# Performance work log

Hardware: AMD Instinct MI355X
Metric: run time of the kernel (lower is better)

The kernel has to match this reference:

```python
import jax, jax.numpy as jnp
import numpy as np

B, IN_CHS, P = 512, 200, 19
CF, TF, K, D, NC = 64, 32, 48, 32, 16
BN_EPS = 1e-5


def _conv(x, w, b=None, dil=1):
    y = jax.lax.conv_general_dilated(x, w, (1, 1), 'VALID',
                                     rhs_dilation=(dil, dil),
                                     dimension_numbers=('NCHW', 'OIHW', 'NCHW'))
    if b is not None:
        y = y + b[None, :, None, None]
    return y


def _upsample_bilinear_ac(x, oh, ow):
    # bilinear with align_corners=True (torch UpsamplingBilinear2d)
    N, C, H, W = x.shape
    ys = jnp.linspace(0.0, H - 1.0, oh)
    xs = jnp.linspace(0.0, W - 1.0, ow)
    y0 = jnp.floor(ys).astype(jnp.int32)
    y1 = jnp.minimum(y0 + 1, H - 1)
    x0 = jnp.floor(xs).astype(jnp.int32)
    x1 = jnp.minimum(x0 + 1, W - 1)
    wy = (ys - y0.astype(ys.dtype))[None, None, :, None]
    wx = (xs - x0.astype(xs.dtype))[None, None, None, :]
    rows = x[:, :, y0, :] * (1.0 - wy) + x[:, :, y1, :] * wy
    return rows[:, :, :, x0] * (1.0 - wx) + rows[:, :, :, x1] * wx


def setup_inputs() -> dict:
    key = jax.random.key(0)
    ks = jax.random.split(key, 24)
    std1 = 1.0 / np.sqrt(K * D)
    inp = {
        'x': jax.random.normal(ks[0], (B, IN_CHS, P, P), jnp.float32),
        'w0': jax.random.normal(ks[1], (CF, IN_CHS, 3, 3), jnp.float32) * 0.02,
        'b0': jnp.zeros((CF,), jnp.float32),
        'w1': jax.random.normal(ks[2], (CF, CF, 3, 3), jnp.float32) * 0.05,
        'b1': jnp.zeros((CF,), jnp.float32),
        'w2': jax.random.normal(ks[3], (CF, CF, 3, 3), jnp.float32) * 0.05,
        'b2': jnp.zeros((CF,), jnp.float32),
        'wa': jax.random.normal(ks[4], (TF, CF, 1, 1), jnp.float32) * 0.08,
        'wb': jax.random.normal(ks[5], (TF, CF, 1, 1), jnp.float32) * 0.08,
        'wg': jax.random.normal(ks[6], (TF, CF, 1, 1), jnp.float32) * 0.08,
        'wd': jax.random.normal(ks[7], (CF, TF, 1, 1), jnp.float32) * 0.08,
        'wenc': jax.random.normal(ks[8], (D, CF, 1, 1), jnp.float32) * 0.08,
        'codewords': jax.random.uniform(ks[9], (K, D), jnp.float32, -std1, std1),
        'scale': jax.random.uniform(ks[10], (K,), jnp.float32, -1.0, 0.0),
        'w_att': jax.random.normal(ks[11], (CF, D), jnp.float32) * 0.1,
        'b_att': jnp.zeros((CF,), jnp.float32),
        'bn_g': jnp.ones((K,), jnp.float32),
        'bn_b': jnp.zeros((K,), jnp.float32),
        'w_d1': jax.random.normal(ks[12], (256, 3 * CF * P * P), jnp.float32) * 0.004,
        'b_d1': jnp.zeros((256,), jnp.float32),
        'w_d2': jax.random.normal(ks[13], (128, 256), jnp.float32) * 0.06,
        'b_d2': jnp.zeros((128,), jnp.float32),
        'w_d3': jax.random.normal(ks[14], (NC, 128), jnp.float32) * 0.09,
        'b_d3': jnp.zeros((NC,), jnp.float32),
    }
    return inp


def reference(x, w0, b0, w1, b1, w2, b2, wa, wb, wg, wd, wenc,
              codewords, scale, w_att, b_att, bn_g, bn_b,
              w_d1, b_d1, w_d2, b_d2, w_d3, b_d3):
    relu = jax.nn.relu
    Hin, Win = x.shape[2], x.shape[3]
    c1 = relu(_conv(x, w0, b0, 1))        # (b, CF, 17, 17)
    c2 = relu(_conv(c1, w1, b1, 2))       # (b, CF, 13, 13)
    xx = relu(_conv(c2, w2, b2, 3))       # (b, CF, 7, 7)
    n, c, h, w = xx.shape
    hw = h * w
    # non-local block; alpha view(n,-1,TF) is a RAW reshape in torch (not a transpose)
    alpha = _conv(xx, wa).reshape(n, hw, TF)
    beta = _conv(xx, wb).reshape(n, TF, hw)
    gam = relu(_conv(xx, wg)).reshape(n, TF, hw)
    ctx = jnp.matmul(alpha, beta)                 # (n, hw, hw)
    ctx = jax.nn.softmax(ctx, axis=0)             # torch F.softmax default dim for 3D tensor is 0
    ctx = jnp.matmul(gam, ctx).reshape(n, TF, h, w)
    ctx = _upsample_bilinear_ac(ctx, h, w)        # same-size -> identity, kept for fidelity
    xx = relu(_conv(ctx, wd)) + xx
    # soft VQ encoding
    Z = relu(_conv(xx, wenc)).reshape(n, D, hw).transpose(0, 2, 1)   # (b, hw, D)
    dist = scale * (jnp.sum(Z * Z, -1, keepdims=True)
                    + jnp.sum(codewords * codewords, -1)[None, None, :]
                    - 2.0 * jnp.einsum('bnd,kd->bnk', Z, codewords))  # (b, hw, K)
    A = jax.nn.softmax(dist, axis=2)
    # E[b,k,d] = sum_n A[b,n,k] * (Z[b,n,d] - C[k,d])
    E = jnp.einsum('bnk,bnd->bkd', A, Z) - A.sum(1)[:, :, None] * codewords[None]
    # BatchNorm1d(K) in training mode: stats over (batch, D) per code k
    mu = E.mean(axis=(0, 2), keepdims=True)
    var = E.var(axis=(0, 2), keepdims=True)
    En = relu((E - mu) / jnp.sqrt(var + BN_EPS) * bn_g[None, :, None] + bn_b[None, :, None])
    E_sum = En.sum(1)                              # (b, D)
    gate = jax.nn.sigmoid(E_sum @ w_att.T + b_att)  # (b, CF)
    xx = xx + xx * gate[:, :, None, None]
    ctx3 = _upsample_bilinear_ac(xx, Hin, Win)
    c2u = _upsample_bilinear_ac(c2, Hin, Win)
    c1u = _upsample_bilinear_ac(c1, Hin, Win)
    feat = jnp.concatenate((c1u, c2u, ctx3), axis=1).reshape(n, -1)  # (b, 69312)
    h1 = relu(feat @ w_d1.T + b_d1)
    h2 = relu(h1 @ w_d2.T + b_d2)
    return h2 @ w_d3.T + b_d3
```

## Files before the change

### kernel.cpp

```cpp
#include <hip/hip_runtime.h>
#include <math.h>


typedef __attribute__((ext_vector_type(8))) short short8v;
typedef __attribute__((ext_vector_type(4))) float f32x4;

#define OFF_WE1H  188928u
#define OFF_WE1L  2556416u
#define OFF_WE2H  4923904u
#define OFF_WE2L  6308352u
#define OFF_WE3H  7692800u
#define OFF_WE3L  8094208u
#define OFF_C1    8495616u
#define OFF_C2    17965568u
#define OFF_XX1   23503360u
#define OFF_ALPHA 25108992u
#define OFF_BETA  25911808u
#define OFF_GAM   26714624u
#define OFF_CTX   27517440u
#define OFF_CTX2  28746752u
#define OFF_XX2   29549568u
#define OFF_Z     31155200u
#define OFF_A     31958016u
#define OFF_E     33162240u
#define OFF_BNS   33948672u
#define OFF_XX3   33948768u
#define OFF_H1    35554400u
#define OFF_H2    35685472u

#define OFF_H1P   OFF_ALPHA
#define OFF_MS    OFF_BETA

#define OFF_WH    OFF_ALPHA
#define OFF_WL    (OFF_ALPHA + 64512u)
#define OFF_W1H   (OFF_ALPHA + 129024u)
#define OFF_W1L   (OFF_W1H + 18432u)
#define OFF_W2H   (OFF_W1L + 18432u)
#define OFF_W2L   (OFF_W2H + 18432u)

__device__ __forceinline__ unsigned bf16_rne_bits(float v) {
    unsigned u = __float_as_uint(v);
    return (u + 0x7FFFu + ((u >> 16) & 1u)) >> 16;
}

__global__ __launch_bounds__(256) void sac_wsplit(const float* __restrict__ w0,
                                                  unsigned short* __restrict__ WH,
                                                  unsigned short* __restrict__ WL) {
    int idx = blockIdx.x * 256 + threadIdx.x;
    if (idx >= 129024) return;
    int ic = idx % 224;
    int c  = (idx / 224) % 64;
    int s  = idx / (224 * 64);
    int ky = s / 3, kx = s % 3;
    float v = 0.f;
    if (ic < 200) v = w0[((c * 200 + ic) * 3 + ky) * 3 + kx];
    unsigned hb = bf16_rne_bits(v);
    float hf = __uint_as_float(hb << 16);
    unsigned lb = bf16_rne_bits(v - hf);
    WH[idx] = (unsigned short)hb;
    WL[idx] = (unsigned short)lb;
}

__global__ __launch_bounds__(256) void sac_wsplit64(const float* __restrict__ wsrc,
                                                    unsigned short* __restrict__ WHo,
                                                    unsigned short* __restrict__ WLo) {
    int idx = blockIdx.x * 256 + threadIdx.x;
    if (idx >= 36864) return;
    int ic = idx & 63;
    int c  = (idx >> 6) & 63;
    int s  = idx >> 12;
    int ky = s / 3, kx = s - ky * 3;
    float v = wsrc[((c * 64 + ic) * 3 + ky) * 3 + kx];
    unsigned hb = bf16_rne_bits(v);
    float hf = __uint_as_float(hb << 16);
    unsigned lb = bf16_rne_bits(v - hf);
    WHo[idx] = (unsigned short)hb;
    WLo[idx] = (unsigned short)lb;
}

__global__ __launch_bounds__(256) void sac_upA(const float* __restrict__ w_d1,
                                               float* __restrict__ tmp, int S, int co) {
    int idx = blockIdx.x * 256 + threadIdx.x;
    int total = 256 * 64 * 19 * S;
    if (idx >= total) return;
    int xp = idx % S;
    int j  = (idx / S) % 19;
    int c  = (idx / (S * 19)) % 64;
    int o  = idx / (S * 19 * 64);
    const float* wrow = w_d1 + (size_t)o * 69312 + (size_t)(co + c) * 361 + j * 19;
    float ratio = (float)(S - 1) / 18.0f;
    float s = 0.f;
    for (int i = 0; i < 19; ++i) {
        float xs = i * ratio;
        int x0 = (int)floorf(xs);
        float wx = xs - (float)x0;
        int x1 = x0 + 1; if (x1 > S - 1) x1 = S - 1;
        float cf = (xp == x0 ? 1.f - wx : 0.f) + (xp == x1 ? wx : 0.f);
        s += cf * wrow[i];
    }
    tmp[idx] = s;
}
__global__ __launch_bounds__(256) void sac_upB_bf16(const float* __restrict__ tmp,
                                                    unsigned short* __restrict__ WEH,
                                                    unsigned short* __restrict__ WEL, int S) {
    int idx = blockIdx.x * 256 + threadIdx.x;
    int total = 256 * 64 * S * S;
    if (idx >= total) return;
    int xp = idx % S;
    int yp = (idx / S) % S;
    int c  = (idx / (S * S)) % 64;
    int o  = idx / (S * S * 64);
    const float* tp = tmp + (((size_t)o * 64 + c) * 19) * S + xp;
    float ratio = (float)(S - 1) / 18.0f;
    float s = 0.f;
    for (int j = 0; j < 19; ++j) {
        float ys = j * ratio;
        int y0 = (int)floorf(ys);
        float wy = ys - (float)y0;
        int y1 = y0 + 1; if (y1 > S - 1) y1 = S - 1;
        float cf = (yp == y0 ? 1.f - wy : 0.f) + (yp == y1 ? wy : 0.f);
        s += cf * tp[j * S];
    }
    unsigned hb = bf16_rne_bits(s);
    float hf = __uint_as_float(hb << 16);
    unsigned lb = bf16_rne_bits(s - hf);
    WEH[idx] = (unsigned short)hb;
    WEL[idx] = (unsigned short)lb;
}

template<int IW, int OW, int DIL, int TOTCH, int WSTR, int NMT, int NIRMAX>
__global__ __launch_bounds__(256, 4) void sac_convmfma(const float* __restrict__ x,
                                                       const unsigned short* __restrict__ WHp,
                                                       const unsigned short* __restrict__ WLp,
                                                       const float* __restrict__ bias,
                                                       float* __restrict__ out) {
    constexpr int OP = OW * OW;
    constexpr int ISZ = IW * IW;
    constexpr int NCHUNK = WSTR / 32;
    constexpr int NRC = NIRMAX * IW;
    constexpr int RB = (NRC + 31) / 32;
    __shared__ __align__(16) unsigned short XH[NRC * 32 + 64];
    __shared__ __align__(16) unsigned short XL[NRC * 32 + 64];
    int blk = blockIdx.x;
    int b = blk / NMT, mt = blk - b * NMT;
    int tid = threadIdx.x;
    int wv = tid >> 6, l = tid & 63;
    int lh = l >> 5, li = l & 31;
    int wm = wv >> 1, wn = wv & 1;
    int q = l >> 4, r = l & 15;
    int p_base = mt * 64 + wm * 32;
    int n_base = wn * 32;
    int pixA = p_base + r;      if (pixA > OP - 1) pixA = OP - 1;
    int pixB = p_base + 16 + r; if (pixB > OP - 1) pixB = OP - 1;
    int pyA = pixA / OW, pxa = pixA - pyA * OW;
    int pyB = pixB / OW, pxb = pixB - pyB * OW;
    int ir0 = (mt * 64) / OW;
    int rcA0 = (pyA - ir0) * IW + pxa;
    int rcB0 = (pyB - ir0) * IW + pxb;

    f32x4 acc[2][2];
    #pragma unroll
    for (int i = 0; i < 2; ++i)
        #pragma unroll
        for (int j = 0; j < 2; ++j) { acc[i][j].x = 0.f; acc[i][j].y = 0.f; acc[i][j].z = 0.f; acc[i][j].w = 0.f; }

    for (int cc = 0; cc < NCHUNK; ++cc) {
        int ch0 = cc * 32;
        __syncthreads();
        for (int it = wv; it < 4 * RB; it += 4) {
            int cg = it / RB, rb = it - cg * RB;
            int rc = rb * 32 + li;
            if (rc < NRC) {
                int chl4 = cg * 2 + lh;
                int ch = ch0 + chl4 * 4;
                int idx = ir0 * IW + rc; if (idx > ISZ - 1) idx = ISZ - 1;
                const float* gp = x + (size_t)b * (TOTCH * ISZ) + (size_t)ch * ISZ + idx;
                float v0 = (ch + 0 < TOTCH) ? gp[0] : 0.f;
                float v1 = (ch + 1 < TOTCH) ? gp[ISZ] : 0.f;
                float v2 = (ch + 2 < TOTCH) ? gp[2 * ISZ] : 0.f;
                float v3 = (ch + 3 < TOTCH) ? gp[3 * ISZ] : 0.f;
                unsigned h0 = bf16_rne_bits(v0); unsigned l0 = bf16_rne_bits(v0 - __uint_as_float(h0 << 16));
                unsigned h1 = bf16_rne_bits(v1); unsigned l1 = bf16_rne_bits(v1 - __uint_as_float(h1 << 16));
                unsigned h2 = bf16_rne_bits(v2); unsigned l2 = bf16_rne_bits(v2 - __uint_as_float(h2 << 16));
                unsigned h3 = bf16_rne_bits(v3); unsigned l3 = bf16_rne_bits(v3 - __uint_as_float(h3 << 16));
                unsigned bo = ((unsigned)(rc * 64 + chl4 * 8)) ^ (unsigned)((rc & 7) << 4);
                uint2 hv; hv.x = h0 | (h1 << 16); hv.y = h2 | (h3 << 16);
                uint2 lv; lv.x = l0 | (l1 << 16); lv.y = l2 | (l3 << 16);
                *(uint2*)((char*)XH + bo) = hv;
                *(uint2*)((char*)XL + bo) = lv;
            }
        }
        __syncthreads();
        #pragma unroll 3
        for (int s9 = 0; s9 < 9; ++s9) {
            int ky = s9 / 3, kx = s9 - ky * 3;
            int rcA = rcA0 + DIL * (ky * IW + kx);
            int rcB = rcB0 + DIL * (ky * IW + kx);
            unsigned byA = ((unsigned)(rcA * 64 + q * 16)) ^ (unsigned)((rcA & 7) << 4);
            unsigned byB = ((unsigned)(rcB * 64 + q * 16)) ^ (unsigned)((rcB & 7) << 4);
            short8v ah0 = *(const short8v*)((const char*)XH + byA);
            short8v al0 = *(const short8v*)((const char*)XL + byA);
            short8v ah1 = *(const short8v*)((const char*)XH + byB);
            short8v al1 = *(const short8v*)((const char*)XL + byB);
            const unsigned short* pWH = WHp + (size_t)(s9 * 64 + n_base + r) * WSTR + ch0 + q * 8;
            const unsigned short* pWL = WLp + (size_t)(s9 * 64 + n_base + r) * WSTR + ch0 + q * 8;
            short8v bh0 = *(const short8v*)(pWH);
            short8v bh1 = *(const short8v*)(pWH + 16 * WSTR);
            short8v bl0 = *(const short8v*)(pWL);
            short8v bl1 = *(const short8v*)(pWL + 16 * WSTR);
            acc[0][0] = __builtin_amdgcn_mfma_f32_16x16x32_bf16(ah0, bh0, acc[0][0], 0, 0, 0);
            acc[0][1] = __builtin_amdgcn_mfma_f32_16x16x32_bf16(ah0, bh1, acc[0][1], 0, 0, 0);
            acc[1][0] = __builtin_amdgcn_mfma_f32_16x16x32_bf16(ah1, bh0, acc[1][0], 0, 0, 0);
            acc[1][1] = __builtin_amdgcn_mfma_f32_16x16x32_bf16(ah1, bh1, acc[1][1], 0, 0, 0);
            acc[0][0] = __builtin_amdgcn_mfma_f32_16x16x32_bf16(ah0, bl0, acc[0][0], 0, 0, 0);
            acc[0][1] = __builtin_amdgcn_mfma_f32_16x16x32_bf16(ah0, bl1, acc[0][1], 0, 0, 0);
            acc[1][0] = __builtin_amdgcn_mfma_f32_16x16x32_bf16(ah1, bl0, acc[1][0], 0, 0, 0);
            acc[1][1] = __builtin_amdgcn_mfma_f32_16x16x32_bf16(ah1, bl1, acc[1][1], 0, 0, 0);
            acc[0][0] = __builtin_amdgcn_mfma_f32_16x16x32_bf16(al0, bh0, acc[0][0], 0, 0, 0);
            acc[0][1] = __builtin_amdgcn_mfma_f32_16x16x32_bf16(al0, bh1, acc[0][1], 0, 0, 0);
            acc[1][0] = __builtin_amdgcn_mfma_f32_16x16x32_bf16(al1, bh0, acc[1][0], 0, 0, 0);
            acc[1][1] = __builtin_amdgcn_mfma_f32_16x16x32_bf16(al1, bh1, acc[1][1], 0, 0, 0);
        }
    }
    float bias0 = bias[n_base + r];
    float bias1 = bias[n_base + 16 + r];
    #pragma unroll
    for (int mf = 0; mf < 2; ++mf) {
        #pragma unroll
        for (int nf = 0; nf < 2; ++nf) {
            int ch = n_base + nf * 16 + r;
            float bs = nf ? bias1 : bias0;
            float* op = out + ((size_t)b * 64 + ch) * OP;
            #pragma unroll
            for (int j = 0; j < 4; ++j) {
                int pix = p_base + mf * 16 + q * 4 + j;
                if (pix < OP) {
                    float v = acc[mf][nf][j] + bs;
                    op[pix] = v > 0.f ? v : 0.f;
                }
            }
        }
    }
}

__global__ __launch_bounds__(256) void sac_abgctx(const float* __restrict__ xx1,
                                                  const float* __restrict__ wa,
                                                  const float* __restrict__ wb,
                                                  const float* __restrict__ wg,
                                                  float* __restrict__ gam,
                                                  float* __restrict__ ctx) {
    int b = blockIdx.x, tid = threadIdx.x;
    __shared__ float xsm[3136];
    __shared__ float ws3[3 * 2048];
    __shared__ float ab[3136];
    for (int f = tid; f < 3136; f += 256) xsm[f] = xx1[(size_t)b * 3136 + f];
    for (int f = tid; f < 2048; f += 256) {
        ws3[f] = wa[f]; ws3[2048 + f] = wb[f]; ws3[4096 + f] = wg[f];
    }
    __syncthreads();
    for (int f = tid; f < 4704; f += 256) {
        int which = f / 1568, r = f - which * 1568;
        int t = r / 49, p = r - t * 49;
        const float* w = &ws3[which * 2048 + t * 64];
        float s = 0.f;
        #pragma unroll 8
        for (int c = 0; c < 64; ++c) s += w[c] * xsm[c * 49 + p];
        if (which == 2) {
            s = s > 0.f ? s : 0.f;
            gam[(size_t)b * 1568 + r] = s;
        } else {
            ab[which * 1568 + r] = s;
        }
    }
    __syncthreads();
    for (int f = tid; f < 2401; f += 256) {
        int i = f / 49, lcol = f - i * 49;
        float s = 0.f;
        #pragma unroll 8
        for (int j = 0; j < 32; ++j) s += ab[i * 32 + j] * ab[1568 + j * 49 + lcol];
        ctx[(size_t)b * 2401 + f] = s;
    }
}

__global__ __launch_bounds__(256) void sac_smstat(const float* __restrict__ ctx,
                                                  float* __restrict__ ms) {
    __shared__ float red[8][32];
    int tid = threadIdx.x;
    int pl = tid & 31, g = tid >> 5;
    int pos = blockIdx.x * 32 + pl;
    bool ok = pos < 2401;
    float m = -1e30f;
    if (ok) for (int b = g; b < 512; b += 8) m = fmaxf(m, ctx[(size_t)b * 2401 + pos]);
    red[g][pl] = m;
    __syncthreads();
    if (g == 0) {
        #pragma unroll
        for (int t = 1; t < 8; ++t) m = fmaxf(m, red[t][pl]);
        red[0][pl] = m;
    }
    __syncthreads();
    m = red[0][pl];
    float s = 0.f;
    if (ok) for (int b = g; b < 512; b += 8) s += expf(ctx[(size_t)b * 2401 + pos] - m);
    __syncthreads();
    red[g][pl] = s;
    __syncthreads();
    if (g == 0 && ok) {
        #pragma unroll
        for (int t = 1; t < 8; ++t) s += red[t][pl];
        ms[pos] = m;
        ms[2401 + pos] = 1.f / s;
    }
}

__global__ __launch_bounds__(256) void sac_ctx2(const float* __restrict__ gam,
                                                const float* __restrict__ ctx,
                                                const float* __restrict__ ms,
                                                float* __restrict__ ctx2) {
    int b = blockIdx.x, tid = threadIdx.x;
    __shared__ float gs[1568];
    __shared__ float cs[2401];
    for (int f = tid; f < 1568; f += 256) gs[f] = gam[(size_t)b * 1568 + f];
    for (int f = tid; f < 2401; f += 256)
        cs[f] = expf(ctx[(size_t)b * 2401 + f] - ms[f]) * ms[2401 + f];
    __syncthreads();
    for (int f = tid; f < 1568; f += 256) {
        int t = f / 49, lcol = f - t * 49;
        float s = 0.f;
        #pragma unroll 7
        for (int i = 0; i < 49; ++i) s += gs[t * 49 + i] * cs[i * 49 + lcol];
        ctx2[(size_t)b * 1568 + f] = s;
    }
}

__global__ __launch_bounds__(256) void sac_xx2z(const float* __restrict__ ctx2,
                                                const float* __restrict__ wd,
                                                const float* __restrict__ xx1,
                                                const float* __restrict__ wenc,
                                                float* __restrict__ xx2,
                                                float* __restrict__ Z) {
    int b = blockIdx.x, tid = threadIdx.x;
    __shared__ float cs[1568];
    __shared__ float wds[2048];
    __shared__ float xs2[3136];
    __shared__ float wt[2048];
    for (int f = tid; f < 1568; f += 256) cs[f] = ctx2[(size_t)b * 1568 + f];
    for (int f = tid; f < 2048; f += 256) {
        wds[f] = wd[f];
        int d = f >> 6, c = f & 63; wt[c * 32 + d] = wenc[f];
    }
    __syncthreads();
    for (int f = tid; f < 3136; f += 256) {
        int c = f / 49, p = f - c * 49;
        float s = 0.f;
        #pragma unroll 8
        for (int t = 0; t < 32; ++t) s += wds[c * 32 + t] * cs[t * 49 + p];
        s = s > 0.f ? s : 0.f;
        s += xx1[(size_t)b * 3136 + f];
        xs2[f] = s;
        xx2[(size_t)b * 3136 + f] = s;
    }
    __syncthreads();
    for (int f = tid; f < 1568; f += 256) {
        int p = f >> 5, d = f & 31;
        float s = 0.f;
        #pragma unroll 8
        for (int c = 0; c < 64; ++c) s += wt[c * 32 + d] * xs2[c * 49 + p];
        Z[(size_t)b * 1568 + f] = s > 0.f ? s : 0.f;
    }
}

__global__ __launch_bounds__(256) void sac_dista(const float* __restrict__ Z,
                                                 const float* __restrict__ cw,
                                                 const float* __restrict__ scale,
                                                 float* __restrict__ A) {
    __shared__ float cws[1536];
    __shared__ float c2s[48];
    __shared__ float scs[48];
    int tid = threadIdx.x;
    for (int f = tid; f < 1536; f += 256) cws[f] = cw[f];
    if (tid < 48) scs[tid] = scale[tid];
    __syncthreads();
    if (tid < 48) {
        float s = 0.f;
        for (int d = 0; d < 32; ++d) { float v = cws[tid * 32 + d]; s += v * v; }
        c2s[tid] = s;
    }
    __syncthreads();
    int idx = blockIdx.x * 256 + tid;
    if (idx >= 25088) return;
    const float4* zp = (const float4*)(Z + (size_t)idx * 32);
    float zr[32];
    #pragma unroll
    for (int q = 0; q < 8; ++q) {
        float4 v = zp[q];
        zr[q * 4] = v.x; zr[q * 4 + 1] = v.y; zr[q * 4 + 2] = v.z; zr[q * 4 + 3] = v.w;
    }
    float z2 = 0.f;
    #pragma unroll
    for (int d = 0; d < 32; ++d) z2 += zr[d] * zr[d];
    float v48[48];
    float m = -1e30f;
    for (int k = 0; k < 48; ++k) {
        float dot = 0.f;
        #pragma unroll
        for (int d = 0; d < 32; ++d) dot += zr[d] * cws[k * 32 + d];
        float dv = scs[k] * (z2 + c2s[k] - 2.f * dot);
        v48[k] = dv;
        m = fmaxf(m, dv);
    }
    float s = 0.f;
    #pragma unroll
    for (int k = 0; k < 48; ++k) { v48[k] = expf(v48[k] - m); s += v48[k]; }
    float inv = 1.f / s;
    float* ap = A + (size_t)idx * 48;
    #pragma unroll
    for (int k = 0; k < 48; ++k) ap[k] = v48[k] * inv;
}

__global__ __launch_bounds__(256) void sac_e(const float* __restrict__ A,
                                             const float* __restrict__ Z,
                                             const float* __restrict__ cw,
                                             float* __restrict__ E) {
    int b = blockIdx.x, tid = threadIdx.x;
    __shared__ float As[2352];
    __shared__ float Zs[1568];
    __shared__ float asum[48];
    for (int f = tid; f < 2352; f += 256) As[f] = A[(size_t)b * 2352 + f];
    for (int f = tid; f < 1568; f += 256) Zs[f] = Z[(size_t)b * 1568 + f];
    __syncthreads();
    if (tid < 48) {
        float s = 0.f;
        for (int p = 0; p < 49; ++p) s += As[p * 48 + tid];
        asum[tid] = s;
    }
    __syncthreads();
    for (int f = tid; f < 1536; f += 256) {
        int k = f >> 5, d = f & 31;
        float s = 0.f;
        #pragma unroll 7
        for (int p = 0; p < 49; ++p) s += As[p * 48 + k] * Zs[p * 32 + d];
        E[(size_t)b * 1536 + f] = s - asum[k] * cw[f];
    }
}

__global__ __launch_bounds__(256) void sac_bnstat(const float* __restrict__ E,
                                                  float* __restrict__ bns) {
    int k = blockIdx.x, tid = threadIdx.x;
    __shared__ float sr[4];
    float s = 0.f;
    for (int i = tid; i < 16384; i += 256) {
        int b = i >> 5, d = i & 31;
        s += E[((size_t)b * 48 + k) * 32 + d];
    }
    #pragma unroll
    for (int off = 32; off > 0; off >>= 1) s += __shfl_xor(s, off, 64);
    int lane = tid & 63, wid = tid >> 6;
    if (lane == 0) sr[wid] = s;
    __syncthreads();
    float mu = (sr[0] + sr[1] + sr[2] + sr[3]) / 16384.f;
    float q = 0.f;
    for (int i = tid; i < 16384; i += 256) {
        int b = i >> 5, d = i & 31;
        float v = E[((size_t)b * 48 + k) * 32 + d] - mu;
        q += v * v;
    }
    #pragma unroll
    for (int off = 32; off > 0; off >>= 1) q += __shfl_xor(q, off, 64);
    __syncthreads();
    if (lane == 0) sr[wid] = q;
    __syncthreads();
    if (tid == 0) {
        float var = (sr[0] + sr[1] + sr[2] + sr[3]) / 16384.f;
        bns[k] = mu;
        bns[48 + k] = rsqrtf(var + 1e-5f);
    }
}

__global__ __launch_bounds__(256) void sac_gate(const float* __restrict__ E,
                                                const float* __restrict__ bns,
                                                const float* __restrict__ bn_g,
                                                const float* __restrict__ bn_b,
                                                const float* __restrict__ w_att,
                                                const float* __restrict__ b_att,
                                                const float* __restrict__ xx2,
                                                float* __restrict__ xx3) {
    int b = blockIdx.x, tid = threadIdx.x;
    __shared__ float esd[32];
    __shared__ float gs[64];
    if (tid < 32) {
        int d = tid;
        float s = 0.f;
        for (int k = 0; k < 48; ++k) {
            float v = (E[((size_t)b * 48 + k) * 32 + d] - bns[k]) * bns[48 + k] * bn_g[k] + bn_b[k];
            s += v > 0.f ? v : 0.f;
        }
        esd[d] = s;
    }
    __syncthreads();
    if (tid < 64) {
        int c = tid;
        float a = b_att[c];
        #pragma unroll 8
        for (int d = 0; d < 32; ++d) a += esd[d] * w_att[c * 32 + d];
        gs[c] = 1.f / (1.f + expf(-a)) + 1.f;
    }
    __syncthreads();
    for (int f = tid; f < 3136; f += 256) {
        int c = f / 49;
        xx3[(size_t)b * 3136 + f] = xx2[(size_t)b * 3136 + f] * gs[c];
    }
}

__global__ __launch_bounds__(256, 4) void sac_d1gemm_mfma(const float* __restrict__ c1,
                                                          const float* __restrict__ c2,
                                                          const float* __restrict__ xx3,
                                                          const unsigned short* __restrict__ we1h,
                                                          const unsigned short* __restrict__ we1l,
                                                          const unsigned short* __restrict__ we2h,
                                                          const unsigned short* __restrict__ we2l,
                                                          const unsigned short* __restrict__ we3h,
                                                          const unsigned short* __restrict__ we3l,
                                                          float* __restrict__ h1p) {
    constexpr int KCH = 128;
    __shared__ unsigned short AH[64 * KCH + 64];
    int blk = blockIdx.x;
    int g = blk >> 5, r5 = blk & 31;
    int b0 = (r5 >> 2) * 64, o0 = (r5 & 3) * 64;
    const float* Ab; const unsigned short *WHb, *WLb; int astr, klen, kbase;
    if (g < 16)      { int slab = g >> 2, kq4 = g & 3;
                       Ab = c1;  WHb = we1h; WLb = we1l; astr = 18496; klen = 1156; kbase = slab * 4624 + kq4 * 1156; }
    else if (g < 24) { int gg = g - 16; int slab = gg >> 2, kq4 = gg & 3;
                       Ab = c2;  WHb = we2h; WLb = we2l; astr = 10816; klen = 1352; kbase = slab * 5408 + kq4 * 1352; }
    else             { int kq4 = g - 24;
                       Ab = xx3; WHb = we3h; WLb = we3l; astr = 3136;  klen = 784;  kbase = kq4 * 784; }
    int tid = threadIdx.x;
    int w = tid >> 6, l = tid & 63;
    int wm = w >> 1, wn = w & 1;
    int q = l >> 4, r = l & 15;

    f32x4 acc[2][2];
    #pragma unroll
    for (int i = 0; i < 2; ++i)
        #pragma unroll
        for (int j = 0; j < 2; ++j) { acc[i][j].x = 0.f; acc[i][j].y = 0.f; acc[i][j].z = 0.f; acc[i][j].w = 0.f; }

    int nkch = (klen + KCH - 1) / KCH;
    for (int kc = 0; kc < nkch; ++kc) {
        int k0 = kc * KCH;
        __syncthreads();
        for (int f = tid; f < 64 * (KCH / 2); f += 256) {
            int row = f >> 6, col2 = (f & 63) << 1;
            int kk = k0 + col2;
            float va = 0.f, vb = 0.f;
            if (kk < klen) {
                float2 v = *(const float2*)(Ab + (size_t)(b0 + row) * astr + kbase + kk);
                va = v.x; vb = v.y;
            }
            unsigned h0 = bf16_rne_bits(va);
            unsigned h1 = bf16_rne_bits(vb);
            unsigned bo = ((unsigned)(row * 256 + col2 * 2)) ^ (unsigned)((row & 7) << 4);
            *(unsigned*)((char*)AH + bo) = h0 | (h1 << 16);
        }
        __syncthreads();
        #pragma unroll
        for (int ks = 0; ks < KCH / 32; ++ks) {
            int k = ks * 32 + q * 8;
            int rowA0 = wm * 32 + r, rowA1 = wm * 32 + 16 + r;
            unsigned byA0 = ((unsigned)(rowA0 * 256 + k * 2)) ^ (unsigned)((rowA0 & 7) << 4);
            unsigned byA1 = ((unsigned)(rowA1 * 256 + k * 2)) ^ (unsigned)((rowA1 & 7) << 4);
            short8v ah0 = *(const short8v*)((const char*)AH + byA0);
            short8v ah1 = *(const short8v*)((const char*)AH + byA1);
            size_t wofs = (size_t)(o0 + wn * 32 + r) * astr + kbase + k0 + k;
            short8v bh0 = *(const short8v*)(WHb + wofs);
            short8v bh1 = *(const short8v*)(WHb + wofs + (size_t)16 * astr);
            short8v bl0 = *(const short8v*)(WLb + wofs);
            short8v bl1 = *(const short8v*)(WLb + wofs + (size_t)16 * astr);
            acc[0][0] = __builtin_amdgcn_mfma_f32_16x16x32_bf16(ah0, bh0, acc[0][0], 0, 0, 0);
            acc[0][1] = __builtin_amdgcn_mfma_f32_16x16x32_bf16(ah0, bh1, acc[0][1], 0, 0, 0);
            acc[1][0] = __builtin_amdgcn_mfma_f32_16x16x32_bf16(ah1, bh0, acc[1][0], 0, 0, 0);
            acc[1][1] = __builtin_amdgcn_mfma_f32_16x16x32_bf16(ah1, bh1, acc[1][1], 0, 0, 0);
            acc[0][0] = __builtin_amdgcn_mfma_f32_16x16x32_bf16(ah0, bl0, acc[0][0], 0, 0, 0);
            acc[0][1] = __builtin_amdgcn_mfma_f32_16x16x32_bf16(ah0, bl1, acc[0][1], 0, 0, 0);
            acc[1][0] = __builtin_amdgcn_mfma_f32_16x16x32_bf16(ah1, bl0, acc[1][0], 0, 0, 0);
            acc[1][1] = __builtin_amdgcn_mfma_f32_16x16x32_bf16(ah1, bl1, acc[1][1], 0, 0, 0);
        }
    }
    #pragma unroll
    for (int mf = 0; mf < 2; ++mf) {
        #pragma unroll
        for (int nf = 0; nf < 2; ++nf) {
            int o = o0 + wn * 32 + nf * 16 + r;
            #pragma unroll
            for (int j = 0; j < 4; ++j) {
                int batch = b0 + wm * 32 + mf * 16 + q * 4 + j;
                h1p[((size_t)g * 512 + batch) * 256 + o] = acc[mf][nf][j];
            }
        }
    }
}

__global__ __launch_bounds__(256) void sac_h1red(const float* __restrict__ h1p,
                                                 const float* __restrict__ b_d1,
                                                 float* __restrict__ h1) {
    int i = blockIdx.x * 256 + threadIdx.x;
    int o = i & 255;
    float s = b_d1[o];
    #pragma unroll
    for (int t = 0; t < 28; ++t) s += h1p[(size_t)t * 131072 + i];
    h1[i] = s > 0.f ? s : 0.f;
}

__global__ __launch_bounds__(256) void sac_h2(const float* __restrict__ h1,
                                              const float* __restrict__ w_d2,
                                              const float* __restrict__ b_d2,
                                              float* __restrict__ h2) {
    int idx = blockIdx.x * 256 + threadIdx.x;
    int b = idx >> 7, o = idx & 127;
    const float* hp = h1 + b * 256;
    const float* wp = w_d2 + o * 256;
    float s = b_d2[o];
    #pragma unroll 4
    for (int k = 0; k < 256; ++k) s += hp[k] * wp[k];
    h2[idx] = s > 0.f ? s : 0.f;
}

__global__ __launch_bounds__(256) void sac_out(const float* __restrict__ h2,
                                               const float* __restrict__ w_d3,
                                               const float* __restrict__ b_d3,
                                               float* __restrict__ out) {
    int idx = blockIdx.x * 256 + threadIdx.x;
    int b = idx >> 4, j = idx & 15;
    const float* hp = h2 + b * 128;
    const float* wp = w_d3 + j * 128;
    float s = b_d3[j];
    #pragma unroll 4
    for (int k = 0; k < 128; ++k) s += hp[k] * wp[k];
    out[idx] = s;
}

extern "C" void kernel_launch(void* const* d_in, const int* in_sizes, int n_in,
                              void* d_out, int out_size, void* d_ws, size_t ws_size,
                              hipStream_t stream) {
    (void)in_sizes; (void)n_in; (void)out_size; (void)ws_size;
    const float* x     = (const float*)d_in[0];
    const float* w0    = (const float*)d_in[1];
    const float* b0    = (const float*)d_in[2];
    const float* w1    = (const float*)d_in[3];
    const float* b1    = (const float*)d_in[4];
    const float* w2    = (const float*)d_in[5];
    const float* b2    = (const float*)d_in[6];
    const float* wa    = (const float*)d_in[7];
    const float* wb    = (const float*)d_in[8];
    const float* wg    = (const float*)d_in[9];
    const float* wd    = (const float*)d_in[10];
    const float* wenc  = (const float*)d_in[11];
    const float* cw    = (const float*)d_in[12];
    const float* scale = (const float*)d_in[13];
    const float* w_att = (const float*)d_in[14];
    const float* b_att = (const float*)d_in[15];
    const float* bn_g  = (const float*)d_in[16];
    const float* bn_b  = (const float*)d_in[17];
    const float* w_d1  = (const float*)d_in[18];
    const float* b_d1  = (const float*)d_in[19];
    const float* w_d2  = (const float*)d_in[20];
    const float* b_d2  = (const float*)d_in[21];
    const float* w_d3  = (const float*)d_in[22];
    const float* b_d3  = (const float*)d_in[23];

    float* ws    = (float*)d_ws;
    unsigned short* WE1H = (unsigned short*)(ws + OFF_WE1H);
    unsigned short* WE1L = (unsigned short*)(ws + OFF_WE1L);
    unsigned short* WE2H = (unsigned short*)(ws + OFF_WE2H);
    unsigned short* WE2L = (unsigned short*)(ws + OFF_WE2L);
    unsigned short* WE3H = (unsigned short*)(ws + OFF_WE3H);
    unsigned short* WE3L = (unsigned short*)(ws + OFF_WE3L);
    float* TMP   = ws + OFF_C1;
    float* C1    = ws + OFF_C1;
    float* C2    = ws + OFF_C2;
    float* XX1   = ws + OFF_XX1;
    float* GAM   = ws + OFF_GAM;
    float* CTX   = ws + OFF_CTX;
    float* H1P   = ws + OFF_H1P;
    float* CTX2  = ws + OFF_CTX2;
    float* XX2   = ws + OFF_XX2;
    float* Z     = ws + OFF_Z;
    float* A     = ws + OFF_A;
    float* E     = ws + OFF_E;
    float* BNS   = ws + OFF_BNS;
    float* XX3   = ws + OFF_XX3;
    float* H1    = ws + OFF_H1;
    float* H2    = ws + OFF_H2;
    float* MS    = ws + OFF_MS;
    unsigned short* WH  = (unsigned short*)(ws + OFF_WH);
    unsigned short* WL  = (unsigned short*)(ws + OFF_WL);
    unsigned short* W1H = (unsigned short*)(ws + OFF_W1H);
    unsigned short* W1L = (unsigned short*)(ws + OFF_W1L);
    unsigned short* W2H = (unsigned short*)(ws + OFF_W2H);
    unsigned short* W2L = (unsigned short*)(ws + OFF_W2L);

    sac_wsplit<<<504, 256, 0, stream>>>(w0, WH, WL);
    sac_wsplit64<<<144, 256, 0, stream>>>(w1, W1H, W1L);
    sac_wsplit64<<<144, 256, 0, stream>>>(w2, W2H, W2L);

    sac_upA<<<20672, 256, 0, stream>>>(w_d1, TMP, 17, 0);
    sac_upB_bf16<<<18496, 256, 0, stream>>>(TMP, WE1H, WE1L, 17);
    sac_upA<<<15808, 256, 0, stream>>>(w_d1, TMP, 13, 64);
    sac_upB_bf16<<<10816, 256, 0, stream>>>(TMP, WE2H, WE2L, 13);
    sac_upA<<<8512, 256, 0, stream>>>(w_d1, TMP, 7, 128);
    sac_upB_bf16<<<3136, 256, 0, stream>>>(TMP, WE3H, WE3L, 7);

    sac_convmfma<19, 17, 1, 200, 224, 5, 7 ><<<2560, 256, 0, stream>>>(x,  WH,  WL,  b0, C1);
    sac_convmfma<17, 13, 2,  64,  64, 3, 10><<<1536, 256, 0, stream>>>(C1, W1H, W1L, b1, C2);
    sac_convmfma<13,  7, 3,  64,  64, 1, 13><<< 512, 256, 0, stream>>>(C2, W2H, W2L, b2, XX1);

    sac_abgctx<<<512, 256, 0, stream>>>(XX1, wa, wb, wg, GAM, CTX);
    sac_smstat<<<76, 256, 0, stream>>>(CTX, MS);
    sac_ctx2<<<512, 256, 0, stream>>>(GAM, CTX, MS, CTX2);
    sac_xx2z<<<512, 256, 0, stream>>>(CTX2, wd, XX1, wenc, XX2, Z);

    sac_dista<<<98, 256, 0, stream>>>(Z, cw, scale, A);
    sac_e<<<512, 256, 0, stream>>>(A, Z, cw, E);
    sac_bnstat<<<48, 256, 0, stream>>>(E, BNS);
    sac_gate<<<512, 256, 0, stream>>>(E, BNS, bn_g, bn_b, w_att, b_att, XX2, XX3);

    sac_d1gemm_mfma<<<896, 256, 0, stream>>>(C1, C2, XX3, WE1H, WE1L, WE2H, WE2L, WE3H, WE3L, H1P);
    sac_h1red<<<512, 256, 0, stream>>>(H1P, b_d1, H1);
    sac_h2<<<256, 256, 0, stream>>>(H1, w_d2, b_d2, H2);
    sac_out<<<32, 256, 0, stream>>>(H2, w_d3, b_d3, (float*)d_out);
}
```

Baseline: 837.0 us.

## Drop low-half bf16 weight split, fuse head MLP, single-pass BN stats

The d1 GEMM weights are now stored only as a single rounded bf16 value instead of a hi/lo pair, which halves the MFMA count and the weight bytes read, and the upsample-fold kernels write one array instead of two. The three head kernels (h1 reduce, d2, d3) are merged into one per-batch kernel that keeps the intermediates in shared memory. BatchNorm statistics are computed in one pass using E[x^2]-mu^2. The precision cut and the one-pass variance both lower numerical accuracy and may push outputs past the tolerance.

```diff
diff --git a/kernel.cpp b/kernel.cpp
--- a/kernel.cpp
+++ b/kernel.cpp
@@ -6,11 +6,8 @@
 typedef __attribute__((ext_vector_type(4))) float f32x4;
 
 #define OFF_WE1H  188928u
-#define OFF_WE1L  2556416u
 #define OFF_WE2H  4923904u
-#define OFF_WE2L  6308352u
 #define OFF_WE3H  7692800u
-#define OFF_WE3L  8094208u
 #define OFF_C1    8495616u
 #define OFF_C2    17965568u
 #define OFF_XX1   23503360u
@@ -101,8 +98,7 @@
     tmp[idx] = s;
 }
 __global__ __launch_bounds__(256) void sac_upB_bf16(const float* __restrict__ tmp,
-                                                    unsigned short* __restrict__ WEH,
-                                                    unsigned short* __restrict__ WEL, int S) {
+                                                    unsigned short* __restrict__ WEH, int S) {
     int idx = blockIdx.x * 256 + threadIdx.x;
     int total = 256 * 64 * S * S;
     if (idx >= total) return;
@@ -121,11 +117,7 @@
         float cf = (yp == y0 ? 1.f - wy : 0.f) + (yp == y1 ? wy : 0.f);
         s += cf * tp[j * S];
     }
-    unsigned hb = bf16_rne_bits(s);
-    float hf = __uint_as_float(hb << 16);
-    unsigned lb = bf16_rne_bits(s - hf);
-    WEH[idx] = (unsigned short)hb;
-    WEL[idx] = (unsigned short)lb;
+    WEH[idx] = (unsigned short)bf16_rne_bits(s);
 }
 
 template<int IW, int OW, int DIL, int TOTCH, int WSTR, int NMT, int NIRMAX>
@@ -447,31 +439,27 @@
 __global__ __launch_bounds__(256) void sac_bnstat(const float* __restrict__ E,
                                                   float* __restrict__ bns) {
     int k = blockIdx.x, tid = threadIdx.x;
-    __shared__ float sr[4];
-    float s = 0.f;
+    __shared__ float sr[4], qr[4];
+    float s = 0.f, q = 0.f;
     for (int i = tid; i < 16384; i += 256) {
         int b = i >> 5, d = i & 31;
-        s += E[((size_t)b * 48 + k) * 32 + d];
-    }
-    #pragma unroll
-    for (int off = 32; off > 0; off >>= 1) s += __shfl_xor(s, off, 64);
+        float v = E[((size_t)b * 48 + k) * 32 + d];
+        s += v;
+        q += v * v;
+    }
+    #pragma unroll
+    for (int off = 32; off > 0; off >>= 1) {
+        s += __shfl_xor(s, off, 64);
+        q += __shfl_xor(q, off, 64);
+    }
     int lane = tid & 63, wid = tid >> 6;
-    if (lane == 0) sr[wid] = s;
-    __syncthreads();
-    float mu = (sr[0] + sr[1] + sr[2] + sr[3]) / 16384.f;
-    float q = 0.f;
-    for (int i = tid; i < 16384; i += 256) {
-        int b = i >> 5, d = i & 31;
-        float v = E[((size_t)b * 48 + k) * 32 + d] - mu;
-        q += v * v;
-    }
-    #pragma unroll
-    for (int off = 32; off > 0; off >>= 1) q += __shfl_xor(q, off, 64);
-    __syncthreads();
-    if (lane == 0) sr[wid] = q;
+    if (lane == 0) { sr[wid] = s; qr[wid] = q; }
     __syncthreads();
     if (tid == 0) {
-        float var = (sr[0] + sr[1] + sr[2] + sr[3]) / 16384.f;
+        float mu = (sr[0] + sr[1] + sr[2] + sr[3]) / 16384.f;
+        float ms2 = (qr[0] + qr[1] + qr[2] + qr[3]) / 16384.f;
+        float var = ms2 - mu * mu;
+        if (var < 0.f) var = 0.f;
         bns[k] = mu;
         bns[48 + k] = rsqrtf(var + 1e-5f);
     }
@@ -516,24 +504,21 @@
                                                           const float* __restrict__ c2,
                                                           const float* __restrict__ xx3,
                                                           const unsigned short* __restrict__ we1h,
-                                                          const unsigned short* __restrict__ we1l,
                                                           const unsigned short* __restrict__ we2h,
-                                                          const unsigned short* __restrict__ we2l,
                                                           const unsigned short* __restrict__ we3h,
-                                                          const unsigned short* __restrict__ we3l,
                                                           float* __restrict__ h1p) {
     constexpr int KCH = 128;
     __shared__ unsigned short AH[64 * KCH + 64];
     int blk = blockIdx.x;
     int g = blk >> 5, r5 = blk & 31;
     int b0 = (r5 >> 2) * 64, o0 = (r5 & 3) * 64;
-    const float* Ab; const unsigned short *WHb, *WLb; int astr, klen, kbase;
+    const float* Ab; const unsigned short *WHb; int astr, klen, kbase;
     if (g < 16)      { int slab = g >> 2, kq4 = g & 3;
-                       Ab = c1;  WHb = we1h; WLb = we1l; astr = 18496; klen = 1156; kbase = slab * 4624 + kq4 * 1156; }
+                       Ab = c1;  WHb = we1h; astr = 18496; klen = 1156; kbase = slab * 4624 + kq4 * 1156; }
     else if (g < 24) { int gg = g - 16; int slab = gg >> 2, kq4 = gg & 3;
-                       Ab = c2;  WHb = we2h; WLb = we2l; astr = 10816; klen = 1352; kbase = slab * 5408 + kq4 * 1352; }
+                       Ab = c2;  WHb = we2h; astr = 10816; klen = 1352; kbase = slab * 5408 + kq4 * 1352; }
     else             { int kq4 = g - 24;
-                       Ab = xx3; WHb = we3h; WLb = we3l; astr = 3136;  klen = 784;  kbase = kq4 * 784; }
+                       Ab = xx3; WHb = we3h; astr = 3136;  klen = 784;  kbase = kq4 * 784; }
     int tid = threadIdx.x;
     int w = tid >> 6, l = tid & 63;
     int wm = w >> 1, wn = w & 1;
@@ -574,16 +559,10 @@
             size_t wofs = (size_t)(o0 + wn * 32 + r) * astr + kbase + k0 + k;
             short8v bh0 = *(const short8v*)(WHb + wofs);
             short8v bh1 = *(const short8v*)(WHb + wofs + (size_t)16 * astr);
-            short8v bl0 = *(const short8v*)(WLb + wofs);
-            short8v bl1 = *(const short8v*)(WLb + wofs + (size_t)16 * astr);
             acc[0][0] = __builtin_amdgcn_mfma_f32_16x16x32_bf16(ah0, bh0, acc[0][0], 0, 0, 0);
             acc[0][1] = __builtin_amdgcn_mfma_f32_16x16x32_bf16(ah0, bh1, acc[0][1], 0, 0, 0);
             acc[1][0] = __builtin_amdgcn_mfma_f32_16x16x32_bf16(ah1, bh0, acc[1][0], 0, 0, 0);
             acc[1][1] = __builtin_amdgcn_mfma_f32_16x16x32_bf16(ah1, bh1, acc[1][1], 0, 0, 0);
-            acc[0][0] = __builtin_amdgcn_mfma_f32_16x16x32_bf16(ah0, bl0, acc[0][0], 0, 0, 0);
-            acc[0][1] = __builtin_amdgcn_mfma_f32_16x16x32_bf16(ah0, bl1, acc[0][1], 0, 0, 0);
-            acc[1][0] = __builtin_amdgcn_mfma_f32_16x16x32_bf16(ah1, bl0, acc[1][0], 0, 0, 0);
-            acc[1][1] = __builtin_amdgcn_mfma_f32_16x16x32_bf16(ah1, bl1, acc[1][1], 0, 0, 0);
         }
     }
     #pragma unroll
@@ -600,43 +579,36 @@
     }
 }
 
-__global__ __launch_bounds__(256) void sac_h1red(const float* __restrict__ h1p,
-                                                 const float* __restrict__ b_d1,
-                                                 float* __restrict__ h1) {
-    int i = blockIdx.x * 256 + threadIdx.x;
-    int o = i & 255;
-    float s = b_d1[o];
-    #pragma unroll
-    for (int t = 0; t < 28; ++t) s += h1p[(size_t)t * 131072 + i];
-    h1[i] = s > 0.f ? s : 0.f;
-}
-
-__global__ __launch_bounds__(256) void sac_h2(const float* __restrict__ h1,
-                                              const float* __restrict__ w_d2,
-                                              const float* __restrict__ b_d2,
-                                              float* __restrict__ h2) {
-    int idx = blockIdx.x * 256 + threadIdx.x;
-    int b = idx >> 7, o = idx & 127;
-    const float* hp = h1 + b * 256;
-    const float* wp = w_d2 + o * 256;
-    float s = b_d2[o];
-    #pragma unroll 4
-    for (int k = 0; k < 256; ++k) s += hp[k] * wp[k];
-    h2[idx] = s > 0.f ? s : 0.f;
-}
-
-__global__ __launch_bounds__(256) void sac_out(const float* __restrict__ h2,
-                                               const float* __restrict__ w_d3,
-                                               const float* __restrict__ b_d3,
-                                               float* __restrict__ out) {
-    int idx = blockIdx.x * 256 + threadIdx.x;
-    int b = idx >> 4, j = idx & 15;
-    const float* hp = h2 + b * 128;
-    const float* wp = w_d3 + j * 128;
-    float s = b_d3[j];
-    #pragma unroll 4
-    for (int k = 0; k < 128; ++k) s += hp[k] * wp[k];
-    out[idx] = s;
+__global__ __launch_bounds__(256) void sac_head(const float* __restrict__ h1p,
+                                                const float* __restrict__ b_d1,
+                                                const float* __restrict__ w_d2,
+                                                const float* __restrict__ b_d2,
+                                                const float* __restrict__ w_d3,
+                                                const float* __restrict__ b_d3,
+                                                float* __restrict__ out) {
+    int b = blockIdx.x, tid = threadIdx.x;
+    __shared__ float h1s[256];
+    __shared__ float h2s[128];
+    float s = b_d1[tid];
+    #pragma unroll
+    for (int t = 0; t < 28; ++t) s += h1p[(size_t)t * 131072 + b * 256 + tid];
+    h1s[tid] = s > 0.f ? s : 0.f;
+    __syncthreads();
+    if (tid < 128) {
+        float s2 = b_d2[tid];
+        const float* wp = w_d2 + tid * 256;
+        #pragma unroll 4
+        for (int k = 0; k < 256; ++k) s2 += h1s[k] * wp[k];
+        h2s[tid] = s2 > 0.f ? s2 : 0.f;
+    }
+    __syncthreads();
+    if (tid < 16) {
+        float s3 = b_d3[tid];
+        const float* wp = w_d3 + tid * 128;
+        #pragma unroll 4
+        for (int k = 0; k < 128; ++k) s3 += h2s[k] * wp[k];
+        out[b * 16 + tid] = s3;
+    }
 }
 
 extern "C" void kernel_launch(void* const* d_in, const int* in_sizes, int n_in,
@@ -670,11 +642,8 @@
 
     float* ws    = (float*)d_ws;
     unsigned short* WE1H = (unsigned short*)(ws + OFF_WE1H);
-    unsigned short* WE1L = (unsigned short*)(ws + OFF_WE1L);
     unsigned short* WE2H = (unsigned short*)(ws + OFF_WE2H);
-    unsigned short* WE2L = (unsigned short*)(ws + OFF_WE2L);
     unsigned short* WE3H = (unsigned short*)(ws + OFF_WE3H);
-    unsigned short* WE3L = (unsigned short*)(ws + OFF_WE3L);
     float* TMP   = ws + OFF_C1;
     float* C1    = ws + OFF_C1;
     float* C2    = ws + OFF_C2;
@@ -689,8 +658,6 @@
     float* E     = ws + OFF_E;
     float* BNS   = ws + OFF_BNS;
     float* XX3   = ws + OFF_XX3;
-    float* H1    = ws + OFF_H1;
-    float* H2    = ws + OFF_H2;
     float* MS    = ws + OFF_MS;
     unsigned short* WH  = (unsigned short*)(ws + OFF_WH);
     unsigned short* WL  = (unsigned short*)(ws + OFF_WL);
@@ -704,11 +671,11 @@
     sac_wsplit64<<<144, 256, 0, stream>>>(w2, W2H, W2L);
 
     sac_upA<<<20672, 256, 0, stream>>>(w_d1, TMP, 17, 0);
-    sac_upB_bf16<<<18496, 256, 0, stream>>>(TMP, WE1H, WE1L, 17);
+    sac_upB_bf16<<<18496, 256, 0, stream>>>(TMP, WE1H, 17);
     sac_upA<<<15808, 256, 0, stream>>>(w_d1, TMP, 13, 64);
-    sac_upB_bf16<<<10816, 256, 0, stream>>>(TMP, WE2H, WE2L, 13);
+    sac_upB_bf16<<<10816, 256, 0, stream>>>(TMP, WE2H, 13);
     sac_upA<<<8512, 256, 0, stream>>>(w_d1, TMP, 7, 128);
-    sac_upB_bf16<<<3136, 256, 0, stream>>>(TMP, WE3H, WE3L, 7);
+    sac_upB_bf16<<<3136, 256, 0, stream>>>(TMP, WE3H, 7);
 
     sac_convmfma<19, 17, 1, 200, 224, 5, 7 ><<<2560, 256, 0, stream>>>(x,  WH,  WL,  b0, C1);
     sac_convmfma<17, 13, 2,  64,  64, 3, 10><<<1536, 256, 0, stream>>>(C1, W1H, W1L, b1, C2);
@@ -724,8 +691,6 @@
     sac_bnstat<<<48, 256, 0, stream>>>(E, BNS);
     sac_gate<<<512, 256, 0, stream>>>(E, BNS, bn_g, bn_b, w_att, b_att, XX2, XX3);
 
-    sac_d1gemm_mfma<<<896, 256, 0, stream>>>(C1, C2, XX3, WE1H, WE1L, WE2H, WE2L, WE3H, WE3L, H1P);
-    sac_h1red<<<512, 256, 0, stream>>>(H1P, b_d1, H1);
-    sac_h2<<<256, 256, 0, stream>>>(H1, w_d2, b_d2, H2);
-    sac_out<<<32, 256, 0, stream>>>(H2, w_d3, b_d3, (float*)d_out);
-}
+    sac_d1gemm_mfma<<<896, 256, 0, stream>>>(C1, C2, XX3, WE1H, WE2H, WE3H, H1P);
+    sac_head<<<512, 256, 0, stream>>>(H1P, b_d1, w_d2, b_d2, w_d3, b_d3, (float*)d_out);
+}
```

New measurement: 789.2 us. 5.7% less time.
